# Kernel tuning notes

Measured on AMD Instinct MI355X. Metric: run time of the kernel, lower is better.

The kernel has to match this reference:

```python
import jax, jax.numpy as jnp
import numpy as np

B, N, D, H = 2, 2048, 1024, 16
DH = D // H  # 64 per-head dim before LRPE
EPS = 1e-5


def setup_inputs() -> dict:
    key = jax.random.key(0)
    ks = jax.random.split(key, 8)
    x = jax.random.normal(ks[0], (B, N, D), dtype=jnp.float32)
    context = jax.random.normal(ks[1], (B, N, D), dtype=jnp.float32)
    Wqkvu = jax.random.normal(ks[2], (4 * D, D), dtype=jnp.float32) * 0.02
    bqkvu = jax.random.normal(ks[3], (4 * D,), dtype=jnp.float32) * 0.02
    Wout = jax.random.normal(ks[4], (D, D), dtype=jnp.float32) * 0.02
    bout = jax.random.normal(ks[5], (D,), dtype=jnp.float32) * 0.02
    # Lrpe theta: 10000**(-2/d * arange(d)) reshaped to (H, 1, DH)
    theta = (10000.0 ** (-2.0 / D * jnp.arange(D, dtype=jnp.float32))).reshape(H, 1, DH)
    ln_w = jnp.ones((D,), dtype=jnp.float32)
    ln_b = jnp.zeros((D,), dtype=jnp.float32)
    return {"x": x, "context": context, "Wqkvu": Wqkvu, "bqkvu": bqkvu,
            "Wout": Wout, "bout": bout, "theta": theta, "ln_w": ln_w, "ln_b": ln_b}


def _lrpe(t, theta, n):
    # t: [b,h,n,d]; theta: [h,1,d]; index: [1,n,1]
    idx = jnp.arange(n, dtype=t.dtype).reshape(1, n, 1)
    th = theta * idx  # [h,n,d]
    return jnp.concatenate([t * jnp.cos(th), t * jnp.sin(th)], axis=-1)  # [b,h,n,2d]


def reference(x, context, Wqkvu, bqkvu, Wout, bout, theta, ln_w, ln_b):
    b, n, d = x.shape
    qkvu = x @ Wqkvu.T + bqkvu  # [b,n,4d]
    q, k, v, u = jnp.split(qkvu, 4, axis=-1)
    tohead = lambda t: t.reshape(b, n, H, DH).transpose(0, 2, 1, 3)  # b h n d
    q, k, v = tohead(q), tohead(k), tohead(v)
    q = jax.nn.silu(q)
    k = jax.nn.silu(k)
    q = _lrpe(q, theta, n)  # [b,h,n,2*DH]
    k = _lrpe(k, theta, n)
    # left form: materialize qk then contract with v
    qk = jnp.einsum('bhmd,bhnd->bhmn', q, k)
    out = jnp.einsum('bhmn,bhne->bhme', qk, v)  # [b,h,n,DH]
    out = out.transpose(0, 2, 1, 3).reshape(b, n, d)
    # LayerNorm
    mu = jnp.mean(out, axis=-1, keepdims=True)
    var = jnp.var(out, axis=-1, keepdims=True)
    out = (out - mu) * jax.lax.rsqrt(var + EPS) * ln_w + ln_b
    out = u * out
    return out @ Wout.T + bout
```

## Files before the change

kernel.cpp:

```cpp
#include <hip/hip_runtime.h>
#include <math.h>

#define B_ 2
#define N_ 2048
#define D_ 1024
#define H_ 16
#define DH_ 64
#define ROWS (B_*N_)
#define FOURD (4*D_)
#define EPS_ 1e-5f

typedef short bf16x8 __attribute__((ext_vector_type(8)));
typedef unsigned short u16x8 __attribute__((ext_vector_type(8)));
typedef float f32x4  __attribute__((ext_vector_type(4)));

typedef const __attribute__((address_space(1))) unsigned int* gp_t;
typedef __attribute__((address_space(3))) unsigned int* lp_t;

__device__ __forceinline__ unsigned short f2bf(float f) {
    unsigned int x = __float_as_uint(f);
    unsigned int r = (x + 0x7fffu + ((x >> 16) & 1u)) >> 16;
    return (unsigned short)r;
}
__device__ __forceinline__ float bf2f(unsigned short u) {
    return __uint_as_float((unsigned int)u << 16);
}

__global__ __launch_bounds__(256)
void cast_table(const float* __restrict__ x, const float* __restrict__ w1,
                const float* __restrict__ w2, const float* __restrict__ theta,
                unsigned short* __restrict__ xb, unsigned short* __restrict__ w1b,
                unsigned short* __restrict__ w2b, unsigned short* __restrict__ cos_t,
                unsigned short* __restrict__ sin_t)
{
    int i = blockIdx.x * 256 + threadIdx.x;
    if (i < 2359296) {
        const float* src; unsigned short* dst; int off;
        if (i < 1048576)      { src = x;  dst = xb;  off = i; }
        else if (i < 2097152) { src = w1; dst = w1b; off = i - 1048576; }
        else                  { src = w2; dst = w2b; off = i - 2097152; }
        float4 v = ((const float4*)src)[off];
        ushort4 o;
        o.x = f2bf(v.x); o.y = f2bf(v.y); o.z = f2bf(v.z); o.w = f2bf(v.w);
        ((ushort4*)dst)[off] = o;
    } else {
        int j  = i - 2359296;
        int n  = j >> 8;
        int c0 = (j & 255) * 4;
        float4 tv = *(const float4*)&theta[c0];
        float t[4] = {tv.x, tv.y, tv.z, tv.w};
        ushort4 co, si;
        unsigned short* cp = (unsigned short*)&co;
        unsigned short* sp = (unsigned short*)&si;
#pragma unroll
        for (int k = 0; k < 4; ++k) {
            float s, c; __sincosf(t[k] * (float)n, &s, &c);
            cp[k] = f2bf(c); sp[k] = f2bf(s);
        }
        *(ushort4*)&cos_t[(size_t)n * D_ + c0] = co;
        *(ushort4*)&sin_t[(size_t)n * D_ + c0] = si;
    }
}

__global__ __launch_bounds__(256)
void gemm_bt_128(const unsigned short* __restrict__ A,
                 const unsigned short* __restrict__ Bw,
                 const float* __restrict__ bias, unsigned short* __restrict__ C,
                 int M, int N, int K, int siluLim)
{
    __shared__ unsigned short As[128 * 64];
    __shared__ unsigned short Bs[128 * 64];

    const int tid  = threadIdx.x;
    const int row0 = blockIdx.y * 128;
    const int col0 = blockIdx.x * 128;
    const int wave = tid >> 6;
    const int lane = tid & 63;
    const int wr   = (wave >> 1) * 64;
    const int wc   = (wave & 1) * 64;
    const int l15  = lane & 15;
    const int quad = lane >> 4;
    const int xr   = l15 & 7;

    f32x4 acc[4][4] = {};

    const int srow = tid >> 3;
    const int skk  = ((tid & 7) ^ (srow & 7)) * 8;
    const unsigned short* ag = A  + (size_t)(row0 + srow) * K + skk;
    const unsigned short* bg = Bw + (size_t)(col0 + srow) * K + skk;
    lp_t asd = (lp_t)(void*)&As[tid * 8];
    lp_t bsd = (lp_t)(void*)&Bs[tid * 8];

    for (int k0 = 0; k0 < K; k0 += 64) {
#pragma unroll
        for (int s = 0; s < 4; ++s) {
            __builtin_amdgcn_global_load_lds((gp_t)(const void*)(ag + (size_t)(32 * s) * K + k0), asd + s * 1024, 16, 0, 0);
            __builtin_amdgcn_global_load_lds((gp_t)(const void*)(bg + (size_t)(32 * s) * K + k0), bsd + s * 1024, 16, 0, 0);
        }
        __syncthreads();

#pragma unroll
        for (int ksub = 0; ksub < 2; ++ksub) {
            const int slot = ((ksub * 4 + quad) ^ xr) * 8;
            bf16x8 af[4], bfr[4];
#pragma unroll
            for (int i = 0; i < 4; ++i)
                af[i] = *(const bf16x8*)&As[(wr + i * 16 + l15) * 64 + slot];
#pragma unroll
            for (int j = 0; j < 4; ++j)
                bfr[j] = *(const bf16x8*)&Bs[(wc + j * 16 + l15) * 64 + slot];
#pragma unroll
            for (int i = 0; i < 4; ++i)
#pragma unroll
                for (int j = 0; j < 4; ++j)
                    acc[i][j] = __builtin_amdgcn_mfma_f32_16x16x32_bf16(af[i], bfr[j], acc[i][j], 0, 0, 0);
        }
        __syncthreads();
    }

#pragma unroll
    for (int i = 0; i < 4; ++i) {
        const int r0 = row0 + wr + i * 16 + quad * 4;
#pragma unroll
        for (int j = 0; j < 4; ++j) {
            const int c = col0 + wc + j * 16 + l15;
            const float bb = bias[c];
#pragma unroll
            for (int r = 0; r < 4; ++r) {
                float v = acc[i][j][r] + bb;
                if (c < siluLim) v = v / (1.f + __expf(-v));
                C[(size_t)(r0 + r) * N + c] = f2bf(v);
            }
        }
    }
}

__global__ __launch_bounds__(256)
void gemm_bt_64(const unsigned short* __restrict__ A,
                const unsigned short* __restrict__ Bw,
                const float* __restrict__ bias, float* __restrict__ C,
                int M, int N, int K)
{
    __shared__ unsigned short As[128 * 64];
    __shared__ unsigned short Bs[64 * 64];

    const int tid  = threadIdx.x;
    const int row0 = blockIdx.y * 128;
    const int col0 = blockIdx.x * 64;
    const int wave = tid >> 6;
    const int lane = tid & 63;
    const int wr   = wave * 32;
    const int l15  = lane & 15;
    const int quad = lane >> 4;
    const int xr   = l15 & 7;

    f32x4 acc[2][4] = {};

    const int srow = tid >> 3;
    const int skk  = ((tid & 7) ^ (srow & 7)) * 8;
    const unsigned short* ag = A  + (size_t)(row0 + srow) * K + skk;
    const unsigned short* bg = Bw + (size_t)(col0 + srow) * K + skk;
    lp_t asd = (lp_t)(void*)&As[tid * 8];
    lp_t bsd = (lp_t)(void*)&Bs[tid * 8];

    for (int k0 = 0; k0 < K; k0 += 64) {
#pragma unroll
        for (int s = 0; s < 4; ++s)
            __builtin_amdgcn_global_load_lds((gp_t)(const void*)(ag + (size_t)(32 * s) * K + k0), asd + s * 1024, 16, 0, 0);
#pragma unroll
        for (int s = 0; s < 2; ++s)
            __builtin_amdgcn_global_load_lds((gp_t)(const void*)(bg + (size_t)(32 * s) * K + k0), bsd + s * 1024, 16, 0, 0);
        __syncthreads();

#pragma unroll
        for (int ksub = 0; ksub < 2; ++ksub) {
            const int slot = ((ksub * 4 + quad) ^ xr) * 8;
            bf16x8 af[2], bfr[4];
#pragma unroll
            for (int i = 0; i < 2; ++i)
                af[i] = *(const bf16x8*)&As[(wr + i * 16 + l15) * 64 + slot];
#pragma unroll
            for (int j = 0; j < 4; ++j)
                bfr[j] = *(const bf16x8*)&Bs[(j * 16 + l15) * 64 + slot];
#pragma unroll
            for (int i = 0; i < 2; ++i)
#pragma unroll
                for (int j = 0; j < 4; ++j)
                    acc[i][j] = __builtin_amdgcn_mfma_f32_16x16x32_bf16(af[i], bfr[j], acc[i][j], 0, 0, 0);
        }
        __syncthreads();
    }

#pragma unroll
    for (int i = 0; i < 2; ++i) {
        const int r0 = row0 + wr + i * 16 + quad * 4;
#pragma unroll
        for (int j = 0; j < 4; ++j) {
            const int c = col0 + j * 16 + l15;
            const float bb = bias[c];
#pragma unroll
            for (int r = 0; r < 4; ++r)
                C[(size_t)(r0 + r) * N + c] = acc[i][j][r] + bb;
        }
    }
}

__global__ __launch_bounds__(256)
void kv_mfma(const unsigned short* __restrict__ qkvu,
             const unsigned short* __restrict__ cos_t,
             const unsigned short* __restrict__ sin_t,
             float* __restrict__ part)
{
    __shared__ unsigned short kl_s[128][136];
    __shared__ unsigned short v_s [64][136];

    const int bid   = blockIdx.x;
    const int chunk = bid & 15;
    const int bh    = bid >> 4;
    const int h     = bh & 15;
    const int b     = bh >> 4;
    const int tid   = threadIdx.x;
    const int lane  = tid & 63;
    const int wave  = tid >> 6;
    const int l15   = lane & 15;
    const int quad  = lane >> 4;
    const int n0    = chunk * 128;

    {
        const int g   = tid & 7;
        const int nn0 = (tid >> 3) * 4;
        ushort4 pc[8], ps[8], pv[8];
#pragma unroll
        for (int r = 0; r < 4; ++r) {
            const int n = n0 + nn0 + r;
            const unsigned short* qrow = qkvu + (size_t)(b * N_ + n) * FOURD;
            u16x8 k8 = *(const u16x8*)(qrow + D_     + h * DH_ + g * 8);
            u16x8 v8 = *(const u16x8*)(qrow + 2 * D_ + h * DH_ + g * 8);
            u16x8 c8 = *(const u16x8*)(cos_t + (size_t)n * D_ + h * DH_ + g * 8);
            u16x8 s8 = *(const u16x8*)(sin_t + (size_t)n * D_ + h * DH_ + g * 8);
#pragma unroll
            for (int j = 0; j < 8; ++j) {
                const float kf = bf2f(k8[j]);
                ((unsigned short*)&pc[j])[r] = f2bf(kf * bf2f(c8[j]));
                ((unsigned short*)&ps[j])[r] = f2bf(kf * bf2f(s8[j]));
                ((unsigned short*)&pv[j])[r] = v8[j];
            }
        }
#pragma unroll
        for (int j = 0; j < 8; ++j) {
            const int dh = g * 8 + j;
            *(ushort4*)&kl_s[dh][nn0]      = pc[j];
            *(ushort4*)&kl_s[64 + dh][nn0] = ps[j];
            *(ushort4*)&v_s[dh][nn0]       = pv[j];
        }
    }
    __syncthreads();

    f32x4 acc[2][4] = {};
#pragma unroll
    for (int ks = 0; ks < 4; ++ks) {
        bf16x8 a0 = *(const bf16x8*)&kl_s[wave * 32 +      l15][ks * 32 + quad * 8];
        bf16x8 a1 = *(const bf16x8*)&kl_s[wave * 32 + 16 + l15][ks * 32 + quad * 8];
#pragma unroll
        for (int j = 0; j < 4; ++j) {
            bf16x8 bfr = *(const bf16x8*)&v_s[j * 16 + l15][ks * 32 + quad * 8];
            acc[0][j] = __builtin_amdgcn_mfma_f32_16x16x32_bf16(a0, bfr, acc[0][j], 0, 0, 0);
            acc[1][j] = __builtin_amdgcn_mfma_f32_16x16x32_bf16(a1, bfr, acc[1][j], 0, 0, 0);
        }
    }

    float* pp = part + ((size_t)bh * 16 + chunk) * 8192;
#pragma unroll
    for (int i = 0; i < 2; ++i) {
        const int d0 = wave * 32 + i * 16 + quad * 4;
#pragma unroll
        for (int j = 0; j < 4; ++j) {
            const int e = j * 16 + l15;
#pragma unroll
            for (int r = 0; r < 4; ++r)
                pp[(d0 + r) * 64 + e] = acc[i][j][r];
        }
    }
}

__global__ __launch_bounds__(256)
void kv_reduce(const float* __restrict__ part, float* __restrict__ kv)
{
    const int i  = blockIdx.x * 256 + threadIdx.x;
    const int bh = i >> 13;
    const float* pp = part + ((size_t)bh * 16) * 8192 + (i & 8191);
    float s = 0.f;
#pragma unroll
    for (int c = 0; c < 16; ++c) s += pp[c * 8192];
    kv[i] = s;
}

__global__ __launch_bounds__(256)
void attn_ln_kernel(const unsigned short* __restrict__ qkvu, const float* __restrict__ kvb,
                    const unsigned short* __restrict__ cos_t,
                    const unsigned short* __restrict__ sin_t,
                    const float* __restrict__ ln_w, const float* __restrict__ ln_b,
                    unsigned short* __restrict__ g)
{
    __shared__ float qc_s[8][1024];
    __shared__ float qs_s[8][1024];
    __shared__ float red[4][16];
    __shared__ float mured[8], rsred[8];

    const int row0 = blockIdx.x * 8;
    const int b    = row0 >> 11;
    const int tid  = threadIdx.x;
    const int lane = tid & 63;
    const int wave = tid >> 6;

    for (int i = tid; i < 2048; i += 256) {
        const int r  = i >> 8;
        const int ci = (i & 255) * 4;
        const int n  = (row0 + r) & (N_ - 1);
        ushort4 qv = *(const ushort4*)&qkvu[(size_t)(row0 + r) * FOURD + ci];
        ushort4 cv = *(const ushort4*)&cos_t[(size_t)n * D_ + ci];
        ushort4 sv = *(const ushort4*)&sin_t[(size_t)n * D_ + ci];
        float4 co, so;
        co.x = bf2f(qv.x) * bf2f(cv.x); so.x = bf2f(qv.x) * bf2f(sv.x);
        co.y = bf2f(qv.y) * bf2f(cv.y); so.y = bf2f(qv.y) * bf2f(sv.y);
        co.z = bf2f(qv.z) * bf2f(cv.z); so.z = bf2f(qv.z) * bf2f(sv.z);
        co.w = bf2f(qv.w) * bf2f(cv.w); so.w = bf2f(qv.w) * bf2f(sv.w);
        *(float4*)&qc_s[r][ci] = co;
        *(float4*)&qs_s[r][ci] = so;
    }
    __syncthreads();

    const int c0 = tid * 4;
    const int h  = c0 >> 6;
    const int e0 = c0 & 63;
    const float* kvp = kvb + (size_t)(b * H_ + h) * 8192;

    float o[8][4] = {};
    for (int d = 0; d < 64; ++d) {
        float4 kc = *(const float4*)&kvp[d * 64 + e0];
        float4 ks = *(const float4*)&kvp[(64 + d) * 64 + e0];
#pragma unroll
        for (int r = 0; r < 8; ++r) {
            const float qc = qc_s[r][h * 64 + d];
            const float qs = qs_s[r][h * 64 + d];
            o[r][0] = fmaf(qc, kc.x, fmaf(qs, ks.x, o[r][0]));
            o[r][1] = fmaf(qc, kc.y, fmaf(qs, ks.y, o[r][1]));
            o[r][2] = fmaf(qc, kc.z, fmaf(qs, ks.z, o[r][2]));
            o[r][3] = fmaf(qc, kc.w, fmaf(qs, ks.w, o[r][3]));
        }
    }

    float sum[8], sq[8];
#pragma unroll
    for (int r = 0; r < 8; ++r) {
        sum[r] = o[r][0] + o[r][1] + o[r][2] + o[r][3];
        sq[r]  = o[r][0]*o[r][0] + o[r][1]*o[r][1] + o[r][2]*o[r][2] + o[r][3]*o[r][3];
    }
#pragma unroll
    for (int off = 32; off; off >>= 1)
#pragma unroll
        for (int r = 0; r < 8; ++r) {
            sum[r] += __shfl_down(sum[r], off, 64);
            sq[r]  += __shfl_down(sq[r],  off, 64);
        }
    if (lane == 0)
#pragma unroll
        for (int r = 0; r < 8; ++r) { red[wave][r] = sum[r]; red[wave][8 + r] = sq[r]; }
    __syncthreads();
    if (tid < 8) {
        const float s  = red[0][tid] + red[1][tid] + red[2][tid] + red[3][tid];
        const float q2 = red[0][8+tid] + red[1][8+tid] + red[2][8+tid] + red[3][8+tid];
        const float mu = s * (1.f / (float)D_);
        const float var = q2 * (1.f / (float)D_) - mu * mu;
        mured[tid] = mu;
        rsred[tid] = rsqrtf(var + EPS_);
    }
    __syncthreads();

    float4 wv = *(const float4*)&ln_w[c0];
    float4 bv = *(const float4*)&ln_b[c0];
#pragma unroll
    for (int r = 0; r < 8; ++r) {
        ushort4 uvb = *(const ushort4*)&qkvu[(size_t)(row0 + r) * FOURD + 3 * D_ + c0];
        const float mu = mured[r], rs = rsred[r];
        ushort4 ov;
        ov.x = f2bf(((o[r][0] - mu) * rs * wv.x + bv.x) * bf2f(uvb.x));
        ov.y = f2bf(((o[r][1] - mu) * rs * wv.y + bv.y) * bf2f(uvb.y));
        ov.z = f2bf(((o[r][2] - mu) * rs * wv.z + bv.z) * bf2f(uvb.z));
        ov.w = f2bf(((o[r][3] - mu) * rs * wv.w + bv.w) * bf2f(uvb.w));
        *(ushort4*)&g[(size_t)(row0 + r) * D_ + c0] = ov;
    }
}

extern "C" void kernel_launch(void* const* d_in, const int* in_sizes, int n_in,
                              void* d_out, int out_size, void* d_ws, size_t ws_size,
                              hipStream_t stream)
{
    const float* x     = (const float*)d_in[0];
    const float* Wqkvu = (const float*)d_in[2];
    const float* bqkvu = (const float*)d_in[3];
    const float* Wout  = (const float*)d_in[4];
    const float* bout  = (const float*)d_in[5];
    const float* theta = (const float*)d_in[6];
    const float* ln_w  = (const float*)d_in[7];
    const float* ln_b  = (const float*)d_in[8];
    float* out = (float*)d_out;

    char* ws = (char*)d_ws;
    unsigned short* qkvu  = (unsigned short*)ws; ws += (size_t)ROWS * FOURD * 2;
    float*          kvbuf = (float*)ws;          ws += (size_t)B_ * H_ * 8192 * 4;
    unsigned short* wqb   = (unsigned short*)ws; ws += (size_t)FOURD * D_ * 2;
    unsigned short* wob   = (unsigned short*)ws; ws += (size_t)D_ * D_ * 2;
    unsigned short* xb    = (unsigned short*)ws; ws += (size_t)ROWS * D_ * 2;
    unsigned short* cost  = (unsigned short*)ws; ws += (size_t)N_ * D_ * 2;
    unsigned short* sint  = (unsigned short*)ws; ws += (size_t)N_ * D_ * 2;
    float*          part  = (float*)ws;
    unsigned short* gb    = (unsigned short*)ws;

    dim3 blk(256);
    cast_table<<<dim3(2883584 / 256), blk, 0, stream>>>(
        x, Wqkvu, Wout, theta, xb, wqb, wob, cost, sint);

    gemm_bt_128<<<dim3(FOURD / 128, ROWS / 128), blk, 0, stream>>>(
        xb, wqb, bqkvu, qkvu, ROWS, FOURD, D_, 2 * D_);
    kv_mfma<<<dim3(32 * 16), blk, 0, stream>>>(qkvu, cost, sint, part);
    kv_reduce<<<dim3(32 * 8192 / 256), blk, 0, stream>>>(part, kvbuf);
    attn_ln_kernel<<<dim3(ROWS / 8), blk, 0, stream>>>(
        qkvu, kvbuf, cost, sint, ln_w, ln_b, gb);
    gemm_bt_64<<<dim3(D_ / 64, ROWS / 128), blk, 0, stream>>>(
        gb, wob, bout, out, ROWS, D_, D_);
}
```

Baseline: 214.2 us.

## Prefetch next GEMM K-tile into registers to overlap loads with MFMA

Both bf16 GEMM kernels stop using direct global-to-LDS loads. They now load the next K-tile into registers while the current tile is being computed, then store those registers to LDS at the top of the next iteration. A custom barrier waits only on the LDS counter (lgkmcnt), so the outstanding global prefetches are not drained at each barrier. Launch bounds are raised to request two blocks per CU. The aim is to hide global memory latency behind the MFMA work, at the cost of extra VGPRs and an explicit register-to-LDS copy.

Result: faster. 205.0 us (-4.3%).

```diff
diff --git a/kernel.cpp b/kernel.cpp
--- a/kernel.cpp
+++ b/kernel.cpp
@@ -14,9 +14,6 @@
 typedef unsigned short u16x8 __attribute__((ext_vector_type(8)));
 typedef float f32x4  __attribute__((ext_vector_type(4)));
 
-typedef const __attribute__((address_space(1))) unsigned int* gp_t;
-typedef __attribute__((address_space(3))) unsigned int* lp_t;
-
 __device__ __forceinline__ unsigned short f2bf(float f) {
     unsigned int x = __float_as_uint(f);
     unsigned int r = (x + 0x7fffu + ((x >> 16) & 1u)) >> 16;
@@ -24,6 +21,11 @@
 }
 __device__ __forceinline__ float bf2f(unsigned short u) {
     return __uint_as_float((unsigned int)u << 16);
+}
+
+__device__ __forceinline__ void bar_lds() {
+    __builtin_amdgcn_s_waitcnt(0xC07F);
+    __builtin_amdgcn_s_barrier();
 }
 
 __global__ __launch_bounds__(256)
@@ -62,7 +64,7 @@
     }
 }
 
-__global__ __launch_bounds__(256)
+__global__ __launch_bounds__(256, 2)
 void gemm_bt_128(const unsigned short* __restrict__ A,
                  const unsigned short* __restrict__ Bw,
                  const float* __restrict__ bias, unsigned short* __restrict__ C,
@@ -88,16 +90,29 @@
     const int skk  = ((tid & 7) ^ (srow & 7)) * 8;
     const unsigned short* ag = A  + (size_t)(row0 + srow) * K + skk;
     const unsigned short* bg = Bw + (size_t)(col0 + srow) * K + skk;
-    lp_t asd = (lp_t)(void*)&As[tid * 8];
-    lp_t bsd = (lp_t)(void*)&Bs[tid * 8];
+
+    u16x8 apre[4], bpre[4];
+#pragma unroll
+    for (int s = 0; s < 4; ++s) {
+        apre[s] = *(const u16x8*)(ag + (size_t)(32 * s) * K);
+        bpre[s] = *(const u16x8*)(bg + (size_t)(32 * s) * K);
+    }
 
     for (int k0 = 0; k0 < K; k0 += 64) {
 #pragma unroll
         for (int s = 0; s < 4; ++s) {
-            __builtin_amdgcn_global_load_lds((gp_t)(const void*)(ag + (size_t)(32 * s) * K + k0), asd + s * 1024, 16, 0, 0);
-            __builtin_amdgcn_global_load_lds((gp_t)(const void*)(bg + (size_t)(32 * s) * K + k0), bsd + s * 1024, 16, 0, 0);
-        }
-        __syncthreads();
+            *(u16x8*)&As[tid * 8 + s * 2048] = apre[s];
+            *(u16x8*)&Bs[tid * 8 + s * 2048] = bpre[s];
+        }
+        bar_lds();
+
+        if (k0 + 64 < K) {
+#pragma unroll
+            for (int s = 0; s < 4; ++s) {
+                apre[s] = *(const u16x8*)(ag + (size_t)(32 * s) * K + k0 + 64);
+                bpre[s] = *(const u16x8*)(bg + (size_t)(32 * s) * K + k0 + 64);
+            }
+        }
 
 #pragma unroll
         for (int ksub = 0; ksub < 2; ++ksub) {
@@ -115,7 +130,7 @@
                 for (int j = 0; j < 4; ++j)
                     acc[i][j] = __builtin_amdgcn_mfma_f32_16x16x32_bf16(af[i], bfr[j], acc[i][j], 0, 0, 0);
         }
-        __syncthreads();
+        bar_lds();
     }
 
 #pragma unroll
@@ -135,7 +150,7 @@
     }
 }
 
-__global__ __launch_bounds__(256)
+__global__ __launch_bounds__(256, 2)
 void gemm_bt_64(const unsigned short* __restrict__ A,
                 const unsigned short* __restrict__ Bw,
                 const float* __restrict__ bias, float* __restrict__ C,
@@ -160,17 +175,32 @@
     const int skk  = ((tid & 7) ^ (srow & 7)) * 8;
     const unsigned short* ag = A  + (size_t)(row0 + srow) * K + skk;
     const unsigned short* bg = Bw + (size_t)(col0 + srow) * K + skk;
-    lp_t asd = (lp_t)(void*)&As[tid * 8];
-    lp_t bsd = (lp_t)(void*)&Bs[tid * 8];
+
+    u16x8 apre[4], bpre[2];
+#pragma unroll
+    for (int s = 0; s < 4; ++s)
+        apre[s] = *(const u16x8*)(ag + (size_t)(32 * s) * K);
+#pragma unroll
+    for (int s = 0; s < 2; ++s)
+        bpre[s] = *(const u16x8*)(bg + (size_t)(32 * s) * K);
 
     for (int k0 = 0; k0 < K; k0 += 64) {
 #pragma unroll
         for (int s = 0; s < 4; ++s)
-            __builtin_amdgcn_global_load_lds((gp_t)(const void*)(ag + (size_t)(32 * s) * K + k0), asd + s * 1024, 16, 0, 0);
+            *(u16x8*)&As[tid * 8 + s * 2048] = apre[s];
 #pragma unroll
         for (int s = 0; s < 2; ++s)
-            __builtin_amdgcn_global_load_lds((gp_t)(const void*)(bg + (size_t)(32 * s) * K + k0), bsd + s * 1024, 16, 0, 0);
-        __syncthreads();
+            *(u16x8*)&Bs[tid * 8 + s * 2048] = bpre[s];
+        bar_lds();
+
+        if (k0 + 64 < K) {
+#pragma unroll
+            for (int s = 0; s < 4; ++s)
+                apre[s] = *(const u16x8*)(ag + (size_t)(32 * s) * K + k0 + 64);
+#pragma unroll
+            for (int s = 0; s < 2; ++s)
+                bpre[s] = *(const u16x8*)(bg + (size_t)(32 * s) * K + k0 + 64);
+        }
 
 #pragma unroll
         for (int ksub = 0; ksub < 2; ++ksub) {
@@ -188,7 +218,7 @@
                 for (int j = 0; j < 4; ++j)
                     acc[i][j] = __builtin_amdgcn_mfma_f32_16x16x32_bf16(af[i], bfr[j], acc[i][j], 0, 0, 0);
         }
-        __syncthreads();
+        bar_lds();
     }
 
 #pragma unroll
```
